# Performance work log

Hardware: AMD Instinct MI355X
Metric: run time of the kernel (lower is better)

Reference implementation:

```python
import jax, jax.numpy as jnp
import numpy as np

TOKENS, IN_DIM, VOCAB = 2048, 2048, 32000
TILE_FACTOR = 16


def setup_inputs() -> dict:
    key = jax.random.key(0)
    k1, k2, k3 = jax.random.split(key, 3)
    inp = jax.random.normal(k1, (TOKENS, IN_DIM), dtype=jnp.float32)
    target = jax.random.randint(k2, (TOKENS,), 0, VOCAB, dtype=jnp.int64)
    # LM-head weight, shape [out_dim(vocab), in_dim] as in nn.Linear
    proj_weight = jax.random.normal(k3, (VOCAB, IN_DIM), dtype=jnp.float32) * 0.02
    return {"input": inp, "target": target, "proj_weight": proj_weight}


def reference(input, target, proj_weight):
    # Original loops over token tiles: for each tile, logits = tile @ W.T,
    # then softmax over vocab (dim=-1). Softmax is per-row (per-token), so the
    # concatenation of per-tile outputs equals the full row-wise softmax.
    # target is accepted but unused, matching the original forward.
    logits = jnp.einsum('td,vd->tv', input, proj_weight)  # [tokens, vocab]
    return jax.nn.softmax(logits, axis=-1)
```

## Files before the change

kernel.cpp:

```cpp
#include <hip/hip_runtime.h>
#include <hip/hip_bf16.h>
#include <math.h>

#define TOKENS 2048
#define IN_DIM 2048
#define VOCAB  32000

#define BM 256
#define BN 256
#define BK 64
#define NKSTEP (IN_DIM / BK)
#define GEMM_GRID ((TOKENS / BM) * (VOCAB / BN))
#define NCT (VOCAB / BN)

typedef short s16x8 __attribute__((ext_vector_type(8)));
typedef float f32x4 __attribute__((ext_vector_type(4)));

__device__ __forceinline__ unsigned short f2bf_rne(float f) {
  unsigned int u = __float_as_uint(f);
  u += 0x7fffu + ((u >> 16) & 1u);
  return (unsigned short)(u >> 16);
}

__global__ __launch_bounds__(256) void convert_f32_to_bf16(
    const float* __restrict__ in, unsigned short* __restrict__ out, int n4) {
  int idx = blockIdx.x * blockDim.x + threadIdx.x;
  int stride = gridDim.x * blockDim.x;
  for (int i = idx; i < n4; i += stride) {
    float4 v = reinterpret_cast<const float4*>(in)[i];
    ushort4 o;
    o.x = f2bf_rne(v.x);
    o.y = f2bf_rne(v.y);
    o.z = f2bf_rne(v.z);
    o.w = f2bf_rne(v.w);
    reinterpret_cast<ushort4*>(out)[i] = o;
  }
}

__device__ __forceinline__ void gload_lds16(const unsigned short* g, unsigned short* l) {
  __builtin_amdgcn_global_load_lds(
      (const __attribute__((address_space(1))) unsigned int*)g,
      (__attribute__((address_space(3))) unsigned int*)l, 16, 0, 0);
}

__global__ __launch_bounds__(512, 2) void gemm_bt(
    const unsigned short* __restrict__ A,
    const unsigned short* __restrict__ B,
    float* __restrict__ C,
    float2* __restrict__ partials) {
  __shared__ __align__(16) unsigned short lds[65536];

  const int tid = threadIdx.x;
  const int lane = tid & 63;
  const int wave = tid >> 6;
  const int wr = wave >> 2;
  const int wc = wave & 3;

  const int bid = blockIdx.x;
  const int lid = (bid & 7) * (GEMM_GRID / 8) + (bid >> 3);
  const int rowTile = lid & 7;
  const int colTile = lid >> 3;
  const int rowBase = rowTile * BM;
  const int colBase = colTile * BN;

  const int r0 = tid >> 3;
  const int r1 = 64 + r0;
  const int c8 = (((tid & 7) ^ (r0 & 7)) << 3);
  const unsigned short* srcA0 = A + (size_t)(rowBase + r0) * IN_DIM + c8;
  const unsigned short* srcA1 = A + (size_t)(rowBase + r1) * IN_DIM + c8;
  const unsigned short* srcB0 = B + (size_t)(colBase + r0) * IN_DIM + c8;
  const unsigned short* srcB1 = B + (size_t)(colBase + r1) * IN_DIM + c8;
  const int ldsD0 = tid * 8;
  const int ldsD1 = (512 + tid) * 8;

  auto stageA = [&](int buf, int h, int k) {
    size_t off = (size_t)h * (128 * IN_DIM) + k;
    int dst = buf * 32768 + h * 8192;
    gload_lds16(srcA0 + off, &lds[dst + ldsD0]);
    gload_lds16(srcA1 + off, &lds[dst + ldsD1]);
  };
  auto stageB = [&](int buf, int h, int k) {
    size_t off = (size_t)h * (128 * IN_DIM) + k;
    int dst = 16384 + buf * 32768 + h * 8192;
    gload_lds16(srcB0 + off, &lds[dst + ldsD0]);
    gload_lds16(srcB1 + off, &lds[dst + ldsD1]);
  };

  const int sc0 = (((lane >> 4) ^ (lane & 7)) << 3);
  const int sc1 = (((4 + (lane >> 4)) ^ (lane & 7)) << 3);
  const int aRow = (wr * 128 + (lane & 15)) * 64;
  const int bRow = 16384 + (wc * 64 + (lane & 15)) * 64;

#define LDA(buf, m, kk) (*(const s16x8*)&lds[(buf) * 32768 + aRow + (m) * 1024 + ((kk) ? sc1 : sc0)])
#define LDB(buf, n, kk) (*(const s16x8*)&lds[(buf) * 32768 + bRow + (n) * 1024 + ((kk) ? sc1 : sc0)])

  f32x4 acc[8][4] = {};

  stageA(0, 0, 0);
  stageA(0, 1, 0);
  stageB(0, 0, 0);
  stageB(0, 1, 0);
  stageA(1, 0, 64);
  stageA(1, 1, 64);
  stageB(1, 0, 64);
  asm volatile("s_waitcnt vmcnt(6)" ::: "memory");
  __builtin_amdgcn_s_barrier();

#define KSTEP(bufc, kn1, kn2)                                                       \
  {                                                                                 \
    s16x8 aL[4][2], aH[4][2], bL[2][2], bH[2][2];                                   \
                                   \
    _Pragma("unroll") for (int m = 0; m < 4; ++m) {                                 \
      aL[m][0] = LDA(bufc, m, 0);                                                   \
      aL[m][1] = LDA(bufc, m, 1);                                                   \
    }                                                                               \
    _Pragma("unroll") for (int n = 0; n < 2; ++n) {                                 \
      bL[n][0] = LDB(bufc, n, 0);                                                   \
      bL[n][1] = LDB(bufc, n, 1);                                                   \
    }                                                                               \
    stageB((bufc) ^ 1, 1, kn1);                                                     \
    asm volatile("s_waitcnt lgkmcnt(8)" ::: "memory");                              \
    __builtin_amdgcn_s_barrier();                                                   \
    asm volatile("s_waitcnt lgkmcnt(0)" ::: "memory");                              \
    __builtin_amdgcn_s_setprio(1);                                                  \
    _Pragma("unroll") for (int m = 0; m < 4; ++m)                                   \
        _Pragma("unroll") for (int n = 0; n < 2; ++n) {                             \
      acc[m][n] = __builtin_amdgcn_mfma_f32_16x16x32_bf16(aL[m][0], bL[n][0], acc[m][n], 0, 0, 0); \
      acc[m][n] = __builtin_amdgcn_mfma_f32_16x16x32_bf16(aL[m][1], bL[n][1], acc[m][n], 0, 0, 0); \
    }                                                                               \
    __builtin_amdgcn_s_setprio(0);                                                  \
    __builtin_amdgcn_s_barrier();                                                   \
                                                      \
    _Pragma("unroll") for (int m = 0; m < 4; ++m) {                                 \
      aH[m][0] = LDA(bufc, 4 + m, 0);                                               \
      aH[m][1] = LDA(bufc, 4 + m, 1);                                               \
    }                                                                               \
    __builtin_amdgcn_s_barrier();                                                   \
    asm volatile("s_waitcnt lgkmcnt(0)" ::: "memory");                              \
    __builtin_amdgcn_s_setprio(1);                                                  \
    _Pragma("unroll") for (int m = 0; m < 4; ++m)                                   \
        _Pragma("unroll") for (int n = 0; n < 2; ++n) {                             \
      acc[4 + m][n] = __builtin_amdgcn_mfma_f32_16x16x32_bf16(aH[m][0], bL[n][0], acc[4 + m][n], 0, 0, 0); \
      acc[4 + m][n] = __builtin_amdgcn_mfma_f32_16x16x32_bf16(aH[m][1], bL[n][1], acc[4 + m][n], 0, 0, 0); \
    }                                                                               \
    __builtin_amdgcn_s_setprio(0);                                                  \
    __builtin_amdgcn_s_barrier();                                                   \
     \
    _Pragma("unroll") for (int n = 0; n < 2; ++n) {                                 \
      bH[n][0] = LDB(bufc, 2 + n, 0);                                               \
      bH[n][1] = LDB(bufc, 2 + n, 1);                                               \
    }                                                                               \
    stageA((bufc), 0, kn2);                                                         \
    stageA((bufc), 1, kn2);                                                         \
    __builtin_amdgcn_s_barrier();                                                   \
    asm volatile("s_waitcnt lgkmcnt(0)" ::: "memory");                              \
    __builtin_amdgcn_s_setprio(1);                                                  \
    _Pragma("unroll") for (int m = 0; m < 4; ++m)                                   \
        _Pragma("unroll") for (int n = 0; n < 2; ++n) {                             \
      acc[4 + m][2 + n] = __builtin_amdgcn_mfma_f32_16x16x32_bf16(aH[m][0], bH[n][0], acc[4 + m][2 + n], 0, 0, 0); \
      acc[4 + m][2 + n] = __builtin_amdgcn_mfma_f32_16x16x32_bf16(aH[m][1], bH[n][1], acc[4 + m][2 + n], 0, 0, 0); \
    }                                                                               \
    __builtin_amdgcn_s_setprio(0);                                                  \
    __builtin_amdgcn_s_barrier();                                                   \
          \
         \
    stageB((bufc), 0, kn2);                                                         \
    __builtin_amdgcn_s_setprio(1);                                                  \
    _Pragma("unroll") for (int m = 0; m < 4; ++m)                                   \
        _Pragma("unroll") for (int n = 0; n < 2; ++n) {                             \
      acc[m][2 + n] = __builtin_amdgcn_mfma_f32_16x16x32_bf16(aL[m][0], bH[n][0], acc[m][2 + n], 0, 0, 0); \
      acc[m][2 + n] = __builtin_amdgcn_mfma_f32_16x16x32_bf16(aL[m][1], bH[n][1], acc[m][2 + n], 0, 0, 0); \
    }                                                                               \
    __builtin_amdgcn_s_setprio(0);                                                  \
    asm volatile("s_waitcnt vmcnt(6)" ::: "memory");                                \
    __builtin_amdgcn_s_barrier();                                                   \
  }

  for (int i = 0; i < NKSTEP / 2; ++i) {
    const int k = i * 128;
    KSTEP(0, (k + 64) & (IN_DIM - 1), (k + 128) & (IN_DIM - 1));
    KSTEP(1, (k + 128) & (IN_DIM - 1), (k + 192) & (IN_DIM - 1));
  }

  asm volatile("s_waitcnt vmcnt(0)" ::: "memory");
  __syncthreads();

#pragma unroll
  for (int m = 0; m < 8; ++m) {
    int row0 = rowBase + wr * 128 + m * 16 + ((lane >> 4) << 2);
#pragma unroll
    for (int n = 0; n < 4; ++n) {
      int col = colBase + wc * 64 + n * 16 + (lane & 15);
#pragma unroll
      for (int j = 0; j < 4; ++j) {
        C[(size_t)(row0 + j) * VOCAB + col] = acc[m][n][j];
      }
    }
  }

  float* lmax = reinterpret_cast<float*>(lds);
  float* lsum = lmax + 1024;
#pragma unroll
  for (int m = 0; m < 8; ++m) {
#pragma unroll
    for (int jj = 0; jj < 4; ++jj) {
      float v0 = acc[m][0][jj], v1 = acc[m][1][jj], v2 = acc[m][2][jj], v3 = acc[m][3][jj];
      float mx = fmaxf(fmaxf(v0, v1), fmaxf(v2, v3));
#pragma unroll
      for (int off = 1; off < 16; off <<= 1) mx = fmaxf(mx, __shfl_xor(mx, off));
      float s = __expf(v0 - mx) + __expf(v1 - mx) + __expf(v2 - mx) + __expf(v3 - mx);
#pragma unroll
      for (int off = 1; off < 16; off <<= 1) s += __shfl_xor(s, off);
      if ((lane & 15) == 0) {
        int r = wr * 128 + m * 16 + ((lane >> 4) << 2) + jj;
        lmax[r * 4 + wc] = mx;
        lsum[r * 4 + wc] = s;
      }
    }
  }
  __syncthreads();
  if (tid < 256) {
    float m0 = lmax[tid * 4 + 0], m1 = lmax[tid * 4 + 1];
    float m2 = lmax[tid * 4 + 2], m3 = lmax[tid * 4 + 3];
    float M = fmaxf(fmaxf(m0, m1), fmaxf(m2, m3));
    float S = lsum[tid * 4 + 0] * __expf(m0 - M) + lsum[tid * 4 + 1] * __expf(m1 - M) +
              lsum[tid * 4 + 2] * __expf(m2 - M) + lsum[tid * 4 + 3] * __expf(m3 - M);
    partials[(size_t)(rowBase + tid) * NCT + colTile] = make_float2(M, S);
  }
#undef LDA
#undef LDB
#undef KSTEP
}

__global__ __launch_bounds__(256) void reduce_stats(
    const float2* __restrict__ partials, float2* __restrict__ stats) {
  int row = blockIdx.x * blockDim.x + threadIdx.x;
  if (row >= TOKENS) return;
  const float2* p = partials + (size_t)row * NCT;
  float M = -3.4e38f, S = 0.f;
  for (int i = 0; i < NCT; ++i) {
    float2 v = p[i];
    if (v.x > M) {
      S *= __expf(M - v.x);
      M = v.x;
    }
    S += v.y * __expf(v.x - M);
  }
  stats[row] = make_float2(M, 1.f / S);
}

__global__ __launch_bounds__(256) void apply_softmax(
    float* __restrict__ C, const float2* __restrict__ stats) {
  const int row = blockIdx.x;
  float* p = C + (size_t)row * VOCAB;
  const float2 st = stats[row];
  const float M = st.x, invS = st.y;
  const int NQ = VOCAB / 4;
  for (int i = threadIdx.x; i < NQ; i += 256) {
    float4 v = reinterpret_cast<const float4*>(p)[i];
    v.x = __expf(v.x - M) * invS;
    v.y = __expf(v.y - M) * invS;
    v.z = __expf(v.z - M) * invS;
    v.w = __expf(v.w - M) * invS;
    reinterpret_cast<float4*>(p)[i] = v;
  }
}

extern "C" void kernel_launch(void* const* d_in, const int* in_sizes, int n_in,
                              void* d_out, int out_size, void* d_ws, size_t ws_size,
                              hipStream_t stream) {
  const float* x = (const float*)d_in[0];
  const float* w = (const float*)d_in[2];
  float* out = (float*)d_out;

  unsigned short* xbf = (unsigned short*)d_ws;
  unsigned short* wbf = xbf + (size_t)TOKENS * IN_DIM;
  float2* partials = (float2*)(wbf + (size_t)VOCAB * IN_DIM);
  float2* stats = partials + (size_t)TOKENS * NCT;

  convert_f32_to_bf16<<<512, 256, 0, stream>>>(x, xbf, TOKENS * IN_DIM / 4);
  convert_f32_to_bf16<<<2048, 256, 0, stream>>>(w, wbf, VOCAB * IN_DIM / 4);
  gemm_bt<<<GEMM_GRID, 512, 0, stream>>>(xbf, wbf, out, partials);
  reduce_stats<<<TOKENS / 256, 256, 0, stream>>>(partials, stats);
  apply_softmax<<<TOKENS, 256, 0, stream>>>(out, stats);
}
```

Before: 485.9 us.

## Make GEMM persistent with cross-tile prefetch and store bf16 shifted logits

Replaces the one-block-per-tile GEMM with a persistent kernel of 256 blocks, each processing 3-4 output tiles. The first loads of the next tile are issued during the last k-steps of the current one, hiding the per-tile prologue and tail. Logits are written as bf16 relative to the tile-local max into the second half of each output row, halving intermediate write and read traffic. The softmax kernel stages each row in LDS before overwriting it in fp32. The cost is reduced precision of the stored logits and tight reliance on the in-place aliasing layout being correct.

```diff
diff --git a/kernel.cpp b/kernel.cpp
--- a/kernel.cpp
+++ b/kernel.cpp
@@ -10,8 +10,9 @@
 #define BN 256
 #define BK 64
 #define NKSTEP (IN_DIM / BK)
-#define GEMM_GRID ((TOKENS / BM) * (VOCAB / BN))
+#define NTILES ((TOKENS / BM) * (VOCAB / BN))
 #define NCT (VOCAB / BN)
+#define PGRID 256
 
 typedef short s16x8 __attribute__((ext_vector_type(8)));
 typedef float f32x4 __attribute__((ext_vector_type(4)));
@@ -20,6 +21,9 @@
   unsigned int u = __float_as_uint(f);
   u += 0x7fffu + ((u >> 16) & 1u);
   return (unsigned short)(u >> 16);
+}
+__device__ __forceinline__ float bf2f(unsigned short h) {
+  return __uint_as_float(((unsigned int)h) << 16);
 }
 
 __global__ __launch_bounds__(256) void convert_f32_to_bf16(
@@ -43,12 +47,15 @@
       (__attribute__((address_space(3))) unsigned int*)l, 16, 0, 0);
 }
 
-__global__ __launch_bounds__(512, 2) void gemm_bt(
+__global__ __launch_bounds__(512, 2) void gemm_persist(
     const unsigned short* __restrict__ A,
     const unsigned short* __restrict__ B,
-    float* __restrict__ C,
+    unsigned short* __restrict__ CB,
     float2* __restrict__ partials) {
   __shared__ __align__(16) unsigned short lds[65536];
+  __shared__ float scrM[1024];
+  __shared__ float scrS[1024];
+  __shared__ float bcastM[256];
 
   const int tid = threadIdx.x;
   const int lane = tid & 63;
@@ -56,34 +63,25 @@
   const int wr = wave >> 2;
   const int wc = wave & 3;
 
-  const int bid = blockIdx.x;
-  const int lid = (bid & 7) * (GEMM_GRID / 8) + (bid >> 3);
-  const int rowTile = lid & 7;
-  const int colTile = lid >> 3;
-  const int rowBase = rowTile * BM;
-  const int colBase = colTile * BN;
+  const int lid0 = (blockIdx.x & 7) * 32 + (blockIdx.x >> 3);
+  const int ntile = (lid0 < NTILES - 3 * PGRID) ? 4 : 3;
 
   const int r0 = tid >> 3;
-  const int r1 = 64 + r0;
   const int c8 = (((tid & 7) ^ (r0 & 7)) << 3);
-  const unsigned short* srcA0 = A + (size_t)(rowBase + r0) * IN_DIM + c8;
-  const unsigned short* srcA1 = A + (size_t)(rowBase + r1) * IN_DIM + c8;
-  const unsigned short* srcB0 = B + (size_t)(colBase + r0) * IN_DIM + c8;
-  const unsigned short* srcB1 = B + (size_t)(colBase + r1) * IN_DIM + c8;
   const int ldsD0 = tid * 8;
   const int ldsD1 = (512 + tid) * 8;
 
-  auto stageA = [&](int buf, int h, int k) {
+  auto stA = [&](int buf, int h, const unsigned short* p0, const unsigned short* p1, int k) {
     size_t off = (size_t)h * (128 * IN_DIM) + k;
     int dst = buf * 32768 + h * 8192;
-    gload_lds16(srcA0 + off, &lds[dst + ldsD0]);
-    gload_lds16(srcA1 + off, &lds[dst + ldsD1]);
+    gload_lds16(p0 + off, &lds[dst + ldsD0]);
+    gload_lds16(p1 + off, &lds[dst + ldsD1]);
   };
-  auto stageB = [&](int buf, int h, int k) {
+  auto stB = [&](int buf, int h, const unsigned short* p0, const unsigned short* p1, int k) {
     size_t off = (size_t)h * (128 * IN_DIM) + k;
     int dst = 16384 + buf * 32768 + h * 8192;
-    gload_lds16(srcB0 + off, &lds[dst + ldsD0]);
-    gload_lds16(srcB1 + off, &lds[dst + ldsD1]);
+    gload_lds16(p0 + off, &lds[dst + ldsD0]);
+    gload_lds16(p1 + off, &lds[dst + ldsD1]);
   };
 
   const int sc0 = (((lane >> 4) ^ (lane & 7)) << 3);
@@ -94,22 +92,29 @@
 #define LDA(buf, m, kk) (*(const s16x8*)&lds[(buf) * 32768 + aRow + (m) * 1024 + ((kk) ? sc1 : sc0)])
 #define LDB(buf, n, kk) (*(const s16x8*)&lds[(buf) * 32768 + bRow + (n) * 1024 + ((kk) ? sc1 : sc0)])
 
-  f32x4 acc[8][4] = {};
-
-  stageA(0, 0, 0);
-  stageA(0, 1, 0);
-  stageB(0, 0, 0);
-  stageB(0, 1, 0);
-  stageA(1, 0, 64);
-  stageA(1, 1, 64);
-  stageB(1, 0, 64);
+  f32x4 acc[8][4];
+
+  int t = lid0;
+  int curRow = (t & 7) * BM, curCol = (t >> 3) * BN;
+  const unsigned short* cA0 = A + (size_t)(curRow + r0) * IN_DIM + c8;
+  const unsigned short* cA1 = cA0 + (size_t)64 * IN_DIM;
+  const unsigned short* cB0 = B + (size_t)(curCol + r0) * IN_DIM + c8;
+  const unsigned short* cB1 = cB0 + (size_t)64 * IN_DIM;
+
+  stA(0, 0, cA0, cA1, 0);
+  stA(0, 1, cA0, cA1, 0);
+  stB(0, 0, cB0, cB1, 0);
+  stB(0, 1, cB0, cB1, 0);
+  stA(1, 0, cA0, cA1, 64);
+  stA(1, 1, cA0, cA1, 64);
+  stB(1, 0, cB0, cB1, 64);
   asm volatile("s_waitcnt vmcnt(6)" ::: "memory");
   __builtin_amdgcn_s_barrier();
 
-#define KSTEP(bufc, kn1, kn2)                                                       \
+#define KSTEP(bufc, kn1, kn2, PB1A, PB1B, PA2A, PA2B, PB2A, PB2B)                   \
   {                                                                                 \
     s16x8 aL[4][2], aH[4][2], bL[2][2], bH[2][2];                                   \
-                                   \
+                                         \
     _Pragma("unroll") for (int m = 0; m < 4; ++m) {                                 \
       aL[m][0] = LDA(bufc, m, 0);                                                   \
       aL[m][1] = LDA(bufc, m, 1);                                                   \
@@ -118,7 +123,7 @@
       bL[n][0] = LDB(bufc, n, 0);                                                   \
       bL[n][1] = LDB(bufc, n, 1);                                                   \
     }                                                                               \
-    stageB((bufc) ^ 1, 1, kn1);                                                     \
+    stB((bufc) ^ 1, 1, PB1A, PB1B, kn1);                                            \
     asm volatile("s_waitcnt lgkmcnt(8)" ::: "memory");                              \
     __builtin_amdgcn_s_barrier();                                                   \
     asm volatile("s_waitcnt lgkmcnt(0)" ::: "memory");                              \
@@ -130,7 +135,7 @@
     }                                                                               \
     __builtin_amdgcn_s_setprio(0);                                                  \
     __builtin_amdgcn_s_barrier();                                                   \
-                                                      \
+                                                                \
     _Pragma("unroll") for (int m = 0; m < 4; ++m) {                                 \
       aH[m][0] = LDA(bufc, 4 + m, 0);                                               \
       aH[m][1] = LDA(bufc, 4 + m, 1);                                               \
@@ -145,13 +150,13 @@
     }                                                                               \
     __builtin_amdgcn_s_setprio(0);                                                  \
     __builtin_amdgcn_s_barrier();                                                   \
-     \
+        \
     _Pragma("unroll") for (int n = 0; n < 2; ++n) {                                 \
       bH[n][0] = LDB(bufc, 2 + n, 0);                                               \
       bH[n][1] = LDB(bufc, 2 + n, 1);                                               \
     }                                                                               \
-    stageA((bufc), 0, kn2);                                                         \
-    stageA((bufc), 1, kn2);                                                         \
+    stA((bufc), 0, PA2A, PA2B, kn2);                                                \
+    stA((bufc), 1, PA2A, PA2B, kn2);                                                \
     __builtin_amdgcn_s_barrier();                                                   \
     asm volatile("s_waitcnt lgkmcnt(0)" ::: "memory");                              \
     __builtin_amdgcn_s_setprio(1);                                                  \
@@ -162,9 +167,8 @@
     }                                                                               \
     __builtin_amdgcn_s_setprio(0);                                                  \
     __builtin_amdgcn_s_barrier();                                                   \
-          \
-         \
-    stageB((bufc), 0, kn2);                                                         \
+       \
+    stB((bufc), 0, PB2A, PB2B, kn2);                                                \
     __builtin_amdgcn_s_setprio(1);                                                  \
     _Pragma("unroll") for (int m = 0; m < 4; ++m)                                   \
         _Pragma("unroll") for (int n = 0; n < 2; ++n) {                             \
@@ -176,56 +180,76 @@
     __builtin_amdgcn_s_barrier();                                                   \
   }
 
-  for (int i = 0; i < NKSTEP / 2; ++i) {
-    const int k = i * 128;
-    KSTEP(0, (k + 64) & (IN_DIM - 1), (k + 128) & (IN_DIM - 1));
-    KSTEP(1, (k + 128) & (IN_DIM - 1), (k + 192) & (IN_DIM - 1));
-  }
-
-  asm volatile("s_waitcnt vmcnt(0)" ::: "memory");
-  __syncthreads();
-
-#pragma unroll
-  for (int m = 0; m < 8; ++m) {
-    int row0 = rowBase + wr * 128 + m * 16 + ((lane >> 4) << 2);
-#pragma unroll
-    for (int n = 0; n < 4; ++n) {
-      int col = colBase + wc * 64 + n * 16 + (lane & 15);
-#pragma unroll
-      for (int j = 0; j < 4; ++j) {
-        C[(size_t)(row0 + j) * VOCAB + col] = acc[m][n][j];
+  for (int ti = 0; ti < ntile; ++ti) {
+    const int curColTile = curCol / BN;
+    const int tn = (ti + 1 < ntile) ? t + PGRID : t;
+    const int nRow = (tn & 7) * BM, nCol = (tn >> 3) * BN;
+    const unsigned short* nA0 = A + (size_t)(nRow + r0) * IN_DIM + c8;
+    const unsigned short* nA1 = nA0 + (size_t)64 * IN_DIM;
+    const unsigned short* nB0 = B + (size_t)(nCol + r0) * IN_DIM + c8;
+    const unsigned short* nB1 = nB0 + (size_t)64 * IN_DIM;
+
+#pragma unroll
+    for (int m = 0; m < 8; ++m)
+#pragma unroll
+      for (int n = 0; n < 4; ++n) acc[m][n] = (f32x4){0.f, 0.f, 0.f, 0.f};
+
+    for (int i = 0; i < 15; ++i) {
+      const int k = i * 128;
+      KSTEP(0, k + 64, k + 128, cB0, cB1, cA0, cA1, cB0, cB1);
+      KSTEP(1, k + 128, k + 192, cB0, cB1, cA0, cA1, cB0, cB1);
+    }
+    KSTEP(0, 1984, 0, cB0, cB1, nA0, nA1, nB0, nB1);
+    KSTEP(1, 0, 64, nB0, nB1, nA0, nA1, nB0, nB1);
+
+#pragma unroll
+    for (int m = 0; m < 8; ++m) {
+#pragma unroll
+      for (int jj = 0; jj < 4; ++jj) {
+        float v0 = acc[m][0][jj], v1 = acc[m][1][jj], v2 = acc[m][2][jj], v3 = acc[m][3][jj];
+        float mx = fmaxf(fmaxf(v0, v1), fmaxf(v2, v3));
+#pragma unroll
+        for (int off = 1; off < 16; off <<= 1) mx = fmaxf(mx, __shfl_xor(mx, off));
+        float s = __expf(v0 - mx) + __expf(v1 - mx) + __expf(v2 - mx) + __expf(v3 - mx);
+#pragma unroll
+        for (int off = 1; off < 16; off <<= 1) s += __shfl_xor(s, off);
+        if ((lane & 15) == 0) {
+          int r = wr * 128 + m * 16 + ((lane >> 4) << 2) + jj;
+          scrM[r * 4 + wc] = mx;
+          scrS[r * 4 + wc] = s;
+        }
       }
     }
-  }
-
-  float* lmax = reinterpret_cast<float*>(lds);
-  float* lsum = lmax + 1024;
-#pragma unroll
-  for (int m = 0; m < 8; ++m) {
-#pragma unroll
-    for (int jj = 0; jj < 4; ++jj) {
-      float v0 = acc[m][0][jj], v1 = acc[m][1][jj], v2 = acc[m][2][jj], v3 = acc[m][3][jj];
-      float mx = fmaxf(fmaxf(v0, v1), fmaxf(v2, v3));
-#pragma unroll
-      for (int off = 1; off < 16; off <<= 1) mx = fmaxf(mx, __shfl_xor(mx, off));
-      float s = __expf(v0 - mx) + __expf(v1 - mx) + __expf(v2 - mx) + __expf(v3 - mx);
-#pragma unroll
-      for (int off = 1; off < 16; off <<= 1) s += __shfl_xor(s, off);
-      if ((lane & 15) == 0) {
-        int r = wr * 128 + m * 16 + ((lane >> 4) << 2) + jj;
-        lmax[r * 4 + wc] = mx;
-        lsum[r * 4 + wc] = s;
+    __syncthreads();
+    if (tid < 256) {
+      float m0 = scrM[tid * 4 + 0], m1 = scrM[tid * 4 + 1];
+      float m2 = scrM[tid * 4 + 2], m3 = scrM[tid * 4 + 3];
+      float M = fmaxf(fmaxf(m0, m1), fmaxf(m2, m3));
+      float S = scrS[tid * 4 + 0] * __expf(m0 - M) + scrS[tid * 4 + 1] * __expf(m1 - M) +
+                scrS[tid * 4 + 2] * __expf(m2 - M) + scrS[tid * 4 + 3] * __expf(m3 - M);
+      partials[(size_t)(curRow + tid) * NCT + curColTile] = make_float2(M, S);
+      bcastM[tid] = M;
+    }
+    __syncthreads();
+#pragma unroll
+    for (int m = 0; m < 8; ++m) {
+#pragma unroll
+      for (int jj = 0; jj < 4; ++jj) {
+        int rloc = wr * 128 + m * 16 + ((lane >> 4) << 2) + jj;
+        float M = bcastM[rloc];
+        unsigned short* cp = CB + (size_t)64000 * (curRow + rloc) + 32000 +
+                             curCol + wc * 64 + (lane & 15);
+#pragma unroll
+        for (int n = 0; n < 4; ++n) cp[n * 16] = f2bf_rne(acc[m][n][jj] - M);
       }
     }
-  }
-  __syncthreads();
-  if (tid < 256) {
-    float m0 = lmax[tid * 4 + 0], m1 = lmax[tid * 4 + 1];
-    float m2 = lmax[tid * 4 + 2], m3 = lmax[tid * 4 + 3];
-    float M = fmaxf(fmaxf(m0, m1), fmaxf(m2, m3));
-    float S = lsum[tid * 4 + 0] * __expf(m0 - M) + lsum[tid * 4 + 1] * __expf(m1 - M) +
-              lsum[tid * 4 + 2] * __expf(m2 - M) + lsum[tid * 4 + 3] * __expf(m3 - M);
-    partials[(size_t)(rowBase + tid) * NCT + colTile] = make_float2(M, S);
+    t = tn;
+    curRow = nRow;
+    curCol = nCol;
+    cA0 = nA0;
+    cA1 = nA1;
+    cB0 = nB0;
+    cB1 = nB1;
   }
 #undef LDA
 #undef LDB
@@ -250,19 +274,32 @@
 }
 
 __global__ __launch_bounds__(256) void apply_softmax(
-    float* __restrict__ C, const float2* __restrict__ stats) {
+    float* __restrict__ Out, const float2* __restrict__ partials,
+    const float2* __restrict__ stats) {
+  __shared__ __align__(16) unsigned short xrow[VOCAB];
   const int row = blockIdx.x;
-  float* p = C + (size_t)row * VOCAB;
+  const unsigned short* src = (const unsigned short*)Out + (size_t)64000 * row + 32000;
+  for (int c = threadIdx.x; c < VOCAB / 8; c += 256)
+    reinterpret_cast<s16x8*>(xrow)[c] = reinterpret_cast<const s16x8*>(src)[c];
+  __syncthreads();
   const float2 st = stats[row];
   const float M = st.x, invS = st.y;
-  const int NQ = VOCAB / 4;
-  for (int i = threadIdx.x; i < NQ; i += 256) {
-    float4 v = reinterpret_cast<const float4*>(p)[i];
-    v.x = __expf(v.x - M) * invS;
-    v.y = __expf(v.y - M) * invS;
-    v.z = __expf(v.z - M) * invS;
-    v.w = __expf(v.w - M) * invS;
-    reinterpret_cast<float4*>(p)[i] = v;
+  const float2* pr = partials + (size_t)row * NCT;
+  float4* dst = reinterpret_cast<float4*>(Out + (size_t)row * VOCAB);
+  for (int c = threadIdx.x; c < VOCAB / 8; c += 256) {
+    s16x8 xv = reinterpret_cast<const s16x8*>(xrow)[c];
+    float base = pr[c >> 5].x - M;
+    float4 o0, o1;
+    o0.x = __expf(bf2f((unsigned short)xv[0]) + base) * invS;
+    o0.y = __expf(bf2f((unsigned short)xv[1]) + base) * invS;
+    o0.z = __expf(bf2f((unsigned short)xv[2]) + base) * invS;
+    o0.w = __expf(bf2f((unsigned short)xv[3]) + base) * invS;
+    o1.x = __expf(bf2f((unsigned short)xv[4]) + base) * invS;
+    o1.y = __expf(bf2f((unsigned short)xv[5]) + base) * invS;
+    o1.z = __expf(bf2f((unsigned short)xv[6]) + base) * invS;
+    o1.w = __expf(bf2f((unsigned short)xv[7]) + base) * invS;
+    dst[c * 2] = o0;
+    dst[c * 2 + 1] = o1;
   }
 }
 
@@ -280,7 +317,7 @@
 
   convert_f32_to_bf16<<<512, 256, 0, stream>>>(x, xbf, TOKENS * IN_DIM / 4);
   convert_f32_to_bf16<<<2048, 256, 0, stream>>>(w, wbf, VOCAB * IN_DIM / 4);
-  gemm_bt<<<GEMM_GRID, 512, 0, stream>>>(xbf, wbf, out, partials);
+  gemm_persist<<<PGRID, 512, 0, stream>>>(xbf, wbf, (unsigned short*)d_out, partials);
   reduce_stats<<<TOKENS / 256, 256, 0, stream>>>(partials, stats);
-  apply_softmax<<<TOKENS, 256, 0, stream>>>(out, stats);
-}
+  apply_softmax<<<TOKENS, 256, 0, stream>>>(out, partials, stats);
+}
```

After: 698.3 us. 43.7% more time.

## Store GEMM logits as bf16 offsets from tile max, staged in output upper half

Applied to the files above, without the earlier changes.

The GEMM epilogue no longer writes fp32 logits. Each block subtracts its per-row tile max and packs the result to bf16 into the upper half of each output row, which halves the intermediate write traffic. apply_softmax copies that bf16 row into LDS, then rebuilds exp(x - M) using the tile max from partials and writes the fp32 probabilities in place. The trade-offs are bf16 precision on logits, a 64 KB LDS buffer per block that limits occupancy in the softmax kernel, and reliance on the in-place aliasing being safe.

```diff
diff --git a/kernel.cpp b/kernel.cpp
--- a/kernel.cpp
+++ b/kernel.cpp
@@ -20,6 +20,9 @@
   unsigned int u = __float_as_uint(f);
   u += 0x7fffu + ((u >> 16) & 1u);
   return (unsigned short)(u >> 16);
+}
+__device__ __forceinline__ float bf2f(unsigned short h) {
+  return __uint_as_float(((unsigned int)h) << 16);
 }
 
 __global__ __launch_bounds__(256) void convert_f32_to_bf16(
@@ -46,7 +49,7 @@
 __global__ __launch_bounds__(512, 2) void gemm_bt(
     const unsigned short* __restrict__ A,
     const unsigned short* __restrict__ B,
-    float* __restrict__ C,
+    unsigned short* __restrict__ CB,
     float2* __restrict__ partials) {
   __shared__ __align__(16) unsigned short lds[65536];
 
@@ -185,21 +188,9 @@
   asm volatile("s_waitcnt vmcnt(0)" ::: "memory");
   __syncthreads();
 
-#pragma unroll
-  for (int m = 0; m < 8; ++m) {
-    int row0 = rowBase + wr * 128 + m * 16 + ((lane >> 4) << 2);
-#pragma unroll
-    for (int n = 0; n < 4; ++n) {
-      int col = colBase + wc * 64 + n * 16 + (lane & 15);
-#pragma unroll
-      for (int j = 0; j < 4; ++j) {
-        C[(size_t)(row0 + j) * VOCAB + col] = acc[m][n][j];
-      }
-    }
-  }
-
   float* lmax = reinterpret_cast<float*>(lds);
   float* lsum = lmax + 1024;
+  float* bM = lmax + 2048;
 #pragma unroll
   for (int m = 0; m < 8; ++m) {
 #pragma unroll
@@ -226,6 +217,36 @@
     float S = lsum[tid * 4 + 0] * __expf(m0 - M) + lsum[tid * 4 + 1] * __expf(m1 - M) +
               lsum[tid * 4 + 2] * __expf(m2 - M) + lsum[tid * 4 + 3] * __expf(m3 - M);
     partials[(size_t)(rowBase + tid) * NCT + colTile] = make_float2(M, S);
+    bM[tid] = M;
+  }
+  __syncthreads();
+
+  const int par = lane & 1;
+  const int e = (lane & 15) & ~1;
+#pragma unroll
+  for (int m = 0; m < 8; ++m) {
+#pragma unroll
+    for (int jj = 0; jj < 4; ++jj) {
+      int rloc = wr * 128 + m * 16 + ((lane >> 4) << 2) + jj;
+      float M = bM[rloc];
+      unsigned int p[4];
+#pragma unroll
+      for (int n = 0; n < 4; ++n) {
+        float v = acc[m][n][jj] - M;
+        float u = __shfl_xor(v, 1);
+        float lo = par ? u : v;
+        float hi = par ? v : u;
+        unsigned int pk;
+        asm("v_cvt_pk_bf16_f32 %0, %1, %2" : "=v"(pk) : "v"(lo), "v"(hi));
+        p[n] = pk;
+      }
+      unsigned int q0 = par ? p[1] : p[0];
+      unsigned int q1 = par ? p[3] : p[2];
+      unsigned short* base = CB + (size_t)64000 * (rowBase + rloc) + 32000 +
+                             colBase + wc * 64;
+      *reinterpret_cast<unsigned int*>(base + 16 * par + e) = q0;
+      *reinterpret_cast<unsigned int*>(base + 32 + 16 * par + e) = q1;
+    }
   }
 #undef LDA
 #undef LDB
@@ -250,19 +271,32 @@
 }
 
 __global__ __launch_bounds__(256) void apply_softmax(
-    float* __restrict__ C, const float2* __restrict__ stats) {
+    float* __restrict__ Out, const float2* __restrict__ partials,
+    const float2* __restrict__ stats) {
+  __shared__ __align__(16) unsigned short xrow[VOCAB];
   const int row = blockIdx.x;
-  float* p = C + (size_t)row * VOCAB;
+  const unsigned short* src = (const unsigned short*)Out + (size_t)64000 * row + 32000;
+  for (int c = threadIdx.x; c < VOCAB / 8; c += 256)
+    reinterpret_cast<s16x8*>(xrow)[c] = reinterpret_cast<const s16x8*>(src)[c];
+  __syncthreads();
   const float2 st = stats[row];
   const float M = st.x, invS = st.y;
-  const int NQ = VOCAB / 4;
-  for (int i = threadIdx.x; i < NQ; i += 256) {
-    float4 v = reinterpret_cast<const float4*>(p)[i];
-    v.x = __expf(v.x - M) * invS;
-    v.y = __expf(v.y - M) * invS;
-    v.z = __expf(v.z - M) * invS;
-    v.w = __expf(v.w - M) * invS;
-    reinterpret_cast<float4*>(p)[i] = v;
+  const float2* pr = partials + (size_t)row * NCT;
+  float4* dst = reinterpret_cast<float4*>(Out + (size_t)row * VOCAB);
+  for (int c = threadIdx.x; c < VOCAB / 8; c += 256) {
+    s16x8 xv = reinterpret_cast<const s16x8*>(xrow)[c];
+    float base = pr[c >> 5].x - M;
+    float4 o0, o1;
+    o0.x = __expf(bf2f((unsigned short)xv[0]) + base) * invS;
+    o0.y = __expf(bf2f((unsigned short)xv[1]) + base) * invS;
+    o0.z = __expf(bf2f((unsigned short)xv[2]) + base) * invS;
+    o0.w = __expf(bf2f((unsigned short)xv[3]) + base) * invS;
+    o1.x = __expf(bf2f((unsigned short)xv[4]) + base) * invS;
+    o1.y = __expf(bf2f((unsigned short)xv[5]) + base) * invS;
+    o1.z = __expf(bf2f((unsigned short)xv[6]) + base) * invS;
+    o1.w = __expf(bf2f((unsigned short)xv[7]) + base) * invS;
+    dst[c * 2] = o0;
+    dst[c * 2 + 1] = o1;
   }
 }
 
@@ -280,7 +314,7 @@
 
   convert_f32_to_bf16<<<512, 256, 0, stream>>>(x, xbf, TOKENS * IN_DIM / 4);
   convert_f32_to_bf16<<<2048, 256, 0, stream>>>(w, wbf, VOCAB * IN_DIM / 4);
-  gemm_bt<<<GEMM_GRID, 512, 0, stream>>>(xbf, wbf, out, partials);
+  gemm_bt<<<GEMM_GRID, 512, 0, stream>>>(xbf, wbf, (unsigned short*)d_out, partials);
   reduce_stats<<<TOKENS / 256, 256, 0, stream>>>(partials, stats);
-  apply_softmax<<<TOKENS, 256, 0, stream>>>(out, stats);
-}
+  apply_softmax<<<TOKENS, 256, 0, stream>>>(out, partials, stats);
+}
```

New measurement: 484.5 us. About the same (-0.3%).
